# Performance work log

Hardware: AMD Instinct MI355X
Metric: run time of the kernel (lower is better)

The kernel has to match this reference:

```python
import jax, jax.numpy as jnp
import numpy as np

N, E, G = 50000, 800000, 64
IN_NODE, OUT_NODE, IN_EDGE = 16, 20, 16
HID_E, N_ACT, HID_C = 64, 8, 256
BN_EPS = 1e-5


def setup_inputs() -> dict:
    key = jax.random.key(0)
    ks = jax.random.split(key, 12)
    def w(i, shape, scale=0.05):
        return jax.random.normal(ks[i], shape, jnp.float32) * scale
    return {
        "x": jax.random.normal(ks[0], (N, IN_NODE), jnp.float32),
        "edge_attr": jax.random.normal(ks[1], (E, IN_EDGE), jnp.float32),
        "a": jax.random.normal(ks[2], (G, N_ACT), jnp.float32),
        "edge_index": jax.random.randint(ks[3], (2, E), 0, N),
        "batch": jnp.sort(jax.random.randint(ks[4], (N,), 0, G)),
        # edge-conditioning MLP: Lin(16,64) -> BN(64) -> ReLU -> Lin(64, 16*20)
        "W1": w(5, (IN_EDGE, HID_E)), "b1": jnp.zeros((HID_E,), jnp.float32),
        "gamma": jnp.ones((HID_E,), jnp.float32), "beta": jnp.zeros((HID_E,), jnp.float32),
        "W2": w(6, (HID_E, IN_NODE * OUT_NODE)), "b2": jnp.zeros((IN_NODE * OUT_NODE,), jnp.float32),
        # NNConv root weight + bias
        "root_w": w(7, (IN_NODE, OUT_NODE)), "bias": jnp.zeros((OUT_NODE,), jnp.float32),
        # critic head: Lin(20+8,256) -> ReLU -> Lin(256,1)
        "Wc1": w(8, (OUT_NODE + N_ACT, HID_C)), "bc1": jnp.zeros((HID_C,), jnp.float32),
        "Wc2": w(9, (HID_C, 1)), "bc2": jnp.zeros((1,), jnp.float32),
    }


def reference(x, edge_attr, a, W1, b1, gamma, beta, W2, b2, root_w, bias,
              Wc1, bc1, Wc2, bc2, edge_index, batch):
    # edge-conditioning MLP (BatchNorm in training mode: batch stats over edges)
    h = edge_attr @ W1 + b1                              # [E, 64]
    mu = jnp.mean(h, axis=0)
    var = jnp.mean(jnp.square(h - mu), axis=0)           # biased var, as BN fwd
    h = (h - mu) * jax.lax.rsqrt(var + BN_EPS) * gamma + beta
    h = jax.nn.relu(h)
    w_e = (h @ W2 + b2).reshape(E, IN_NODE, OUT_NODE)    # per-edge weight matrix

    src, dst = edge_index[0], edge_index[1]
    msg = jnp.einsum('ei,eio->eo', x[src], w_e)          # gather + per-edge matvec [E, 20]
    aggr = jax.ops.segment_sum(msg, dst, num_segments=N) # scatter-add (NNConv aggr='add')
    out = x @ root_w + aggr + bias                       # [N, 20]

    # global mean pool over graphs
    sums = jax.ops.segment_sum(out, batch, num_segments=G)            # [G, 20]
    cnt = jax.ops.segment_sum(jnp.ones((N, 1), out.dtype), batch, num_segments=G)
    pooled = sums / jnp.maximum(cnt, 1.0)

    z = jnp.concatenate([pooled, a], axis=1)             # [G, 28]
    z = jax.nn.relu(z @ Wc1 + bc1)
    return z @ Wc2 + bc2                                 # [G, 1]
```

## Files before the change

kernel.cpp:

```cpp
#include <hip/hip_runtime.h>


#define E_EDGES   800000
#define N_NODES   50000
#define G_GRAPHS  64
#define EDGE_GRID 6144
#define NGROUPS   50000
#define GSTRIDE   1536
#define NSUP      256
#define STAT_GRID 512
#define QSCALE    131072.0f
#define QINV      (1.0f / 131072.0f)

typedef _Float16 f16x2 __attribute__((ext_vector_type(2)));
typedef _Float16 f16x8 __attribute__((ext_vector_type(8)));
typedef __fp16   fp16x2 __attribute__((ext_vector_type(2)));
typedef float    f32x4 __attribute__((ext_vector_type(4)));
typedef unsigned u32x4 __attribute__((ext_vector_type(4)));

union H2U { f16x2 h; unsigned u; };
union F8U { f16x8 v; f16x2 h2[4]; u32x4 u4; };

__device__ __forceinline__ f16x2 pkrtz(float a, float b) {
  fp16x2 r = __builtin_amdgcn_cvt_pkrtz(a, b);
  return __builtin_bit_cast(f16x2, r);
}

__global__ __launch_bounds__(256) void setup_kernel(
    const float* __restrict__ W2, const float* __restrict__ b2,
    const float* __restrict__ W1, const float* __restrict__ x,
    const float* __restrict__ ea, unsigned* __restrict__ Bbuf,
    unsigned* __restrict__ Bw1, unsigned* __restrict__ xh,
    float* __restrict__ gstatsT)
{
  __shared__ float red[4][272];
  const int b = blockIdx.x, tid = threadIdx.x;
  if (b < STAT_GRID) {
    int lane = tid & 63, wave = tid >> 6;
    int nl = lane & 15, q = lane >> 4;
    int gw = b * 4 + wave;
    f32x4 acc = (f32x4){0.f, 0.f, 0.f, 0.f};
    float ms = 0.f;
    for (int c0 = gw; c0 < E_EDGES / 32; c0 += STAT_GRID * 4) {
      const float* p = ea + (size_t)(c0 * 32 + q * 8) * 16 + nl;
      float v0 = p[0],  v1 = p[16], v2 = p[32], v3 = p[48];
      float v4 = p[64], v5 = p[80], v6 = p[96], v7 = p[112];
      ms += (v0 + v1) + (v2 + v3) + (v4 + v5) + (v6 + v7);
      F8U av;
      av.h2[0] = pkrtz(v0, v1); av.h2[1] = pkrtz(v2, v3);
      av.h2[2] = pkrtz(v4, v5); av.h2[3] = pkrtz(v6, v7);
      acc = __builtin_amdgcn_mfma_f32_16x16x32_f16(av.v, av.v, acc, 0, 0, 0);
    }
    ms += __shfl_xor(ms, 16, 64);
    ms += __shfl_xor(ms, 32, 64);
#pragma unroll
    for (int r = 0; r < 4; ++r) red[wave][(q * 4 + r) * 16 + nl] = acc[r];
    if (q == 0) red[wave][256 + nl] = ms;
    __syncthreads();
    for (int v = tid; v < 272; v += 256)
      gstatsT[(size_t)v * STAT_GRID + b] =
          red[0][v] + red[1][v] + red[2][v] + red[3][v];
  } else if (b < STAT_GRID + 70) {
    int idx = (b - STAT_GRID) * 256 + tid;
    if (idx < 33 * 512) {
      int r = idx & 3, lane = (idx >> 2) & 63, nt = (idx >> 8) & 1,
          s = idx >> 9;
      int q = lane >> 4, nl = lane & 15, n = nt * 16 + nl;
      float v0 = 0.f, v1 = 0.f;
      if (n < 20) {
        if (s < 32) {
          int K0 = s * 32 + q * 8 + 2 * r;
          v0 = W2[(K0 >> 4) * 320 + (K0 & 15) * 20 + n];
          v1 = W2[((K0 + 1) >> 4) * 320 + ((K0 + 1) & 15) * 20 + n];
        } else if (q < 2) {
          int i0 = q * 8 + 2 * r;
          v0 = b2[i0 * 20 + n];
          v1 = b2[(i0 + 1) * 20 + n];
        }
      }
      H2U pk; pk.h = pkrtz(v0, v1);
      Bbuf[idx] = pk.u;
    } else {
      int idx2 = idx - 33 * 512;
      int r = idx2 & 3, lane = (idx2 >> 2) & 63, nt = idx2 >> 8;
      int q = lane >> 4, nl = lane & 15, n = nt * 16 + nl;
      int k0 = q * 8 + 2 * r;
      float v0 = (k0 < 16)     ? W1[k0 * 64 + n]       : 0.f;
      float v1 = (k0 + 1 < 16) ? W1[(k0 + 1) * 64 + n] : 0.f;
      H2U pk; pk.h = pkrtz(v0, v1);
      Bw1[idx2] = pk.u;
    }
  } else {
    int i = (b - STAT_GRID - 70) * 256 + tid;
    if (i < N_NODES * 8) {
      H2U pk; pk.h = pkrtz(x[2 * i], x[2 * i + 1]);
      xh[i] = pk.u;
    }
  }
}

__global__ __launch_bounds__(256) void mid_kernel(
    const float* __restrict__ gstatsT, const float* __restrict__ W1,
    const float* __restrict__ b1, const float* __restrict__ gamma,
    const float* __restrict__ beta, const float* __restrict__ x,
    const int* __restrict__ batch, float* __restrict__ sc,
    float* __restrict__ sh, float* __restrict__ sumx,
    float* __restrict__ cntf)
{
  const int t = threadIdx.x;
  if (blockIdx.x == G_GRAPHS) {
    __shared__ float S[272];
    for (int v = t; v < 272; v += 256) {
      const float* p = gstatsT + (size_t)v * STAT_GRID;
      float s0 = 0.f, s1 = 0.f, s2 = 0.f, s3 = 0.f;
      for (int bb = 0; bb < STAT_GRID; bb += 4) {
        s0 += p[bb]; s1 += p[bb + 1]; s2 += p[bb + 2]; s3 += p[bb + 3];
      }
      S[v] = (s0 + s1) + (s2 + s3);
    }
    __syncthreads();
    if (t < 64) {
      float w[16];
#pragma unroll
      for (int j = 0; j < 16; ++j) w[j] = W1[j * 64 + t];
      const float invE = 1.0f / (float)E_EDGES;
      float mw = 0.f;
#pragma unroll
      for (int j = 0; j < 16; ++j) mw += S[256 + j] * w[j];
      mw *= invE;
      float qf = 0.f;
      for (int j = 0; j < 16; ++j) {
        float tt = 0.f;
#pragma unroll
        for (int j2 = 0; j2 < 16; ++j2) tt += S[j * 16 + j2] * w[j2];
        qf += w[j] * tt;
      }
      qf *= invE;
      float b = b1[t];
      float meanH = mw + b;
      float eh2 = qf + 2.f * b * mw + b * b;
      float var = eh2 - meanH * meanH;
      float s = gamma[t] * rsqrtf(var + 1e-5f);
      sc[t] = s;
      sh[t] = beta[t] + (b - meanH) * s;
    }
  } else {
    int g = blockIdx.x;
    __shared__ int se[2];
    if (t < 2) {
      int key = g + t;
      int lo = 0, hi = N_NODES;
      while (lo < hi) {
        int mid = (lo + hi) >> 1;
        if (batch[mid] < key) lo = mid + 1; else hi = mid;
      }
      se[t] = lo;
    }
    __syncthreads();
    int start = se[0], end = se[1];
    int c = t & 15, rr = t >> 4;
    float s = 0.f;
    for (int n = start + rr; n < end; n += 16) s += x[(size_t)n * 16 + c];
    __shared__ float red[256];
    red[t] = s;
    __syncthreads();
#pragma unroll
    for (int st = 128; st >= 16; st >>= 1) {
      if (t < st) red[t] += red[t + st];
      __syncthreads();
    }
    if (t < 16) sumx[g * 16 + t] = red[t];
    if (t == 0) cntf[g] = (float)(end - start);
  }
}

__global__ __launch_bounds__(64, 3) void edge_kernel(
    const unsigned* __restrict__ xh, const float* __restrict__ ea,
    const int* __restrict__ ei, const int* __restrict__ batch,
    const float* __restrict__ sc, const float* __restrict__ sh,
    const unsigned* __restrict__ Bbuf, const unsigned* __restrict__ Bw1v,
    int* __restrict__ gpartI)
{
  __shared__ unsigned hh[320];
  __shared__ int gacc[1280];
  const int lane = threadIdx.x;
  const int nl = lane & 15, q = lane >> 4;
  const int s = blockIdx.x;
  const int kq = (s >> 3) & 3;
  const int sgroup = ((s >> 5) << 3) | (s & 7);
  const int* srcp = ei;
  const int* dstp = ei + E_EDGES;

  for (int v = lane; v < 1280; v += 64) gacc[v] = 0;

  F8U bb[8][2];
#pragma unroll
  for (int sl = 0; sl < 8; ++sl)
#pragma unroll
    for (int nt = 0; nt < 2; ++nt)
      bb[sl][nt].u4 =
          ((const u32x4*)Bbuf)[((kq * 8 + sl) * 2 + nt) * 64 + lane];
  F8U bx[2];
  if (kq == 3) {
    bx[0].u4 = ((const u32x4*)Bbuf)[64 * 64 + lane];
    bx[1].u4 = ((const u32x4*)Bbuf)[65 * 64 + lane];
  } else {
    bx[0].u4 = (u32x4){0u, 0u, 0u, 0u};
    bx[1].u4 = (u32x4){0u, 0u, 0u, 0u};
  }
  F8U bw1; bw1.u4 = ((const u32x4*)Bw1v)[kq * 64 + lane];
  const float scv = sc[kq * 16 + nl];
  const float shv = sh[kq * 16 + nl];
  const int hrb = (q >> 1) * 20 + nl;
  const int qh = q & 1;

  int g = sgroup;
  f32x4 eaA = (f32x4){0.f,0.f,0.f,0.f}, eaB = eaA;
  u32x4 xp = (u32x4){0u,0u,0u,0u};
  int ge = 0;
  {
    int base = g * 16;
    if (q < 2) {
      const float* p = ea + (size_t)(base + nl) * 16 + q * 8;
      eaA = *(const f32x4*)p;
      eaB = *(const f32x4*)(p + 4);
    }
    int src = srcp[base + nl];
    xp = ((const u32x4*)xh)[src * 2 + qh];
    ge = batch[dstp[base + nl]];
  }

  while (g < NGROUPS) {
    const int gn = g + GSTRIDE;

    {
      F8U aEA;
      if (q < 2) {
        aEA.h2[0] = pkrtz(eaA[0], eaA[1]); aEA.h2[1] = pkrtz(eaA[2], eaA[3]);
        aEA.h2[2] = pkrtz(eaB[0], eaB[1]); aEA.h2[3] = pkrtz(eaB[2], eaB[3]);
      } else {
        aEA.u4 = (u32x4){0u, 0u, 0u, 0u};
      }
      f32x4 hD = __builtin_amdgcn_mfma_f32_16x16x32_f16(
          aEA.v, bw1.v, (f32x4){0.f, 0.f, 0.f, 0.f}, 0, 0, 0);
#pragma unroll
      for (int r = 0; r < 4; ++r) {
        float h = fmaxf(hD[r] * scv + shv, 0.f);
        H2U pk; pk.h = pkrtz(h, h);
        hh[nl * 20 + q * 4 + r] = pk.u;
      }
    }
    F8U xcur; xcur.u4 = xp;
    int gq0 = __shfl(ge, q * 4 + 0, 64);
    int gq1 = __shfl(ge, q * 4 + 1, 64);
    int gq2 = __shfl(ge, q * 4 + 2, 64);
    int gq3 = __shfl(ge, q * 4 + 3, 64);

    f32x4 eaAn = (f32x4){0.f,0.f,0.f,0.f}, eaBn = eaAn;
    u32x4 xpn = (u32x4){0u,0u,0u,0u};
    int gen = 0;
    if (gn < NGROUPS) {
      int base = gn * 16;
      if (q < 2) {
        const float* p = ea + (size_t)(base + nl) * 16 + q * 8;
        eaAn = *(const f32x4*)p;
        eaBn = *(const f32x4*)(p + 4);
      }
      int src = srcp[base + nl];
      xpn = ((const u32x4*)xh)[src * 2 + qh];
      gen = batch[dstp[base + nl]];
    }

    f32x4 acc0 = (f32x4){0.f, 0.f, 0.f, 0.f};
    f32x4 acc1 = (f32x4){0.f, 0.f, 0.f, 0.f};
#pragma unroll
    for (int sl = 0; sl < 8; ++sl) {
      H2U hu; hu.u = hh[hrb + sl * 40];
      F8U av;
      av.h2[0] = hu.h * xcur.h2[0];
      av.h2[1] = hu.h * xcur.h2[1];
      av.h2[2] = hu.h * xcur.h2[2];
      av.h2[3] = hu.h * xcur.h2[3];
      acc0 = __builtin_amdgcn_mfma_f32_16x16x32_f16(av.v, bb[sl][0].v, acc0,
                                                    0, 0, 0);
      acc1 = __builtin_amdgcn_mfma_f32_16x16x32_f16(av.v, bb[sl][1].v, acc1,
                                                    0, 0, 0);
    }
    if (kq == 3) {
      F8U av;
      if (q < 2) av = xcur;
      else       av.u4 = (u32x4){0u, 0u, 0u, 0u};
      acc0 = __builtin_amdgcn_mfma_f32_16x16x32_f16(av.v, bx[0].v, acc0,
                                                    0, 0, 0);
      acc1 = __builtin_amdgcn_mfma_f32_16x16x32_f16(av.v, bx[1].v, acc1,
                                                    0, 0, 0);
    }

    {
      int gi;
      gi = gq0 * 20;
      atomicAdd(&gacc[gi + nl], __float2int_rn(acc0[0] * QSCALE));
      if (nl < 4) atomicAdd(&gacc[gi + 16 + nl], __float2int_rn(acc1[0] * QSCALE));
      gi = gq1 * 20;
      atomicAdd(&gacc[gi + nl], __float2int_rn(acc0[1] * QSCALE));
      if (nl < 4) atomicAdd(&gacc[gi + 16 + nl], __float2int_rn(acc1[1] * QSCALE));
      gi = gq2 * 20;
      atomicAdd(&gacc[gi + nl], __float2int_rn(acc0[2] * QSCALE));
      if (nl < 4) atomicAdd(&gacc[gi + 16 + nl], __float2int_rn(acc1[2] * QSCALE));
      gi = gq3 * 20;
      atomicAdd(&gacc[gi + nl], __float2int_rn(acc0[3] * QSCALE));
      if (nl < 4) atomicAdd(&gacc[gi + 16 + nl], __float2int_rn(acc1[3] * QSCALE));
    }

    g = gn;
    eaA = eaAn; eaB = eaBn; xp = xpn; ge = gen;
  }

  const int ssup = s & (NSUP - 1);
  for (int v = lane; v < 1280; v += 64) {
    int gg = v / 20, o = v - gg * 20;
    atomicAdd(&gpartI[(gg * NSUP + ssup) * 20 + o], gacc[v]);
  }
}

__global__ __launch_bounds__(256) void critic_kernel(
    const int* __restrict__ gpartI, const float* __restrict__ sumx,
    const float* __restrict__ cntf, const float* __restrict__ root_w,
    const float* __restrict__ bias, const float* __restrict__ a,
    const float* __restrict__ Wc1, const float* __restrict__ bc1,
    const float* __restrict__ Wc2, const float* __restrict__ bc2,
    float* __restrict__ out)
{
  int g = blockIdx.x, t = threadIdx.x;
  __shared__ int part[240];
  __shared__ float pooled[20];
  if (t < 240) {
    int col = t % 20, r = t / 20;
    int s = 0;
    const int* gp = gpartI + (size_t)g * NSUP * 20;
    for (int sl = r; sl < NSUP; sl += 12) s += gp[sl * 20 + col];
    part[t] = s;
  }
  __syncthreads();
  if (t < 20) {
    int si = 0;
#pragma unroll
    for (int r = 0; r < 12; ++r) si += part[r * 20 + t];
    float s = (float)si * QINV;
    float cnt = cntf[g];
    float base = bias[t] * cnt;
#pragma unroll
    for (int i = 0; i < 16; ++i) base += sumx[g * 16 + i] * root_w[i * 20 + t];
    pooled[t] = (s + base) / fmaxf(cnt, 1.f);
  }
  __syncthreads();
  float z = bc1[t];
#pragma unroll
  for (int j = 0; j < 20; ++j) z += pooled[j] * Wc1[j * 256 + t];
#pragma unroll
  for (int j = 0; j < 8; ++j) z += a[g * 8 + j] * Wc1[(20 + j) * 256 + t];
  z = fmaxf(z, 0.f);
  float pr = z * Wc2[t];
#pragma unroll
  for (int off = 32; off >= 1; off >>= 1) pr += __shfl_down(pr, off, 64);
  __shared__ float red[4];
  if ((t & 63) == 0) red[t >> 6] = pr;
  __syncthreads();
  if (t == 0) out[g] = red[0] + red[1] + red[2] + red[3] + bc2[0];
}

extern "C" void kernel_launch(void* const* d_in, const int* in_sizes, int n_in,
                              void* d_out, int out_size, void* d_ws,
                              size_t ws_size, hipStream_t stream) {
  const float* x         = (const float*)d_in[0];
  const float* edge_attr = (const float*)d_in[1];
  const float* a         = (const float*)d_in[2];
  const int*   ei        = (const int*)d_in[3];
  const int*   batch     = (const int*)d_in[4];
  const float* W1        = (const float*)d_in[5];
  const float* b1        = (const float*)d_in[6];
  const float* gamma     = (const float*)d_in[7];
  const float* beta      = (const float*)d_in[8];
  const float* W2        = (const float*)d_in[9];
  const float* b2        = (const float*)d_in[10];
  const float* root_w    = (const float*)d_in[11];
  const float* bias      = (const float*)d_in[12];
  const float* Wc1       = (const float*)d_in[13];
  const float* bc1       = (const float*)d_in[14];
  const float* Wc2       = (const float*)d_in[15];
  const float* bc2       = (const float*)d_in[16];
  float* out = (float*)d_out;

  float* wsf     = (float*)d_ws;
  float* sc      = wsf;
  float* sh      = wsf + 64;
  float* sumx    = wsf + 128;
  float* cntf    = wsf + 1152;
  unsigned* Bw1  = (unsigned*)(wsf + 1216);
  unsigned* Bbuf = (unsigned*)(wsf + 2240);
  float* gstatsT = wsf + 19136;
  unsigned* xhp  = (unsigned*)(wsf + 158400);
  int* gpartI    = (int*)(wsf + 558400);

  (void)hipMemsetAsync(gpartI, 0, (size_t)G_GRAPHS * NSUP * 20 * sizeof(int),
                       stream);

  const int XCONV_BLOCKS = (N_NODES * 8 + 255) / 256;
  setup_kernel<<<STAT_GRID + 70 + XCONV_BLOCKS, 256, 0, stream>>>(
      W2, b2, W1, x, edge_attr, Bbuf, Bw1, xhp, gstatsT);
  mid_kernel<<<G_GRAPHS + 1, 256, 0, stream>>>(gstatsT, W1, b1, gamma, beta,
                                               x, batch, sc, sh, sumx, cntf);
  edge_kernel<<<EDGE_GRID, 64, 0, stream>>>(xhp, edge_attr, ei, batch, sc,
                                            sh, Bbuf, Bw1, gpartI);
  critic_kernel<<<G_GRAPHS, 256, 0, stream>>>(gpartI, sumx, cntf, root_w,
                                              bias, a, Wc1, bc1, Wc2, bc2,
                                              out);
}
```

Measured before the change: 252.4 us.

## Software-pipeline edge kernel with double-buffered hidden tile and split MFMA chains

Restructures the edge loop so the hidden activations for the next group are computed one iteration ahead into a double-buffered LDS tile, and global loads are prefetched two groups ahead. The main MFMA accumulation is split into two independent accumulator chains per output tile to shorten dependency chains. Float-to-int quantization uses a magic-number add trick instead of a round conversion. This costs more registers and LDS, which may cut occupancy under the 3-waves bound.

Measured after the change: 239.5 us. 5.1% less time.

```diff
diff --git a/kernel.cpp b/kernel.cpp
--- a/kernel.cpp
+++ b/kernel.cpp
@@ -24,6 +24,11 @@
 __device__ __forceinline__ f16x2 pkrtz(float a, float b) {
   fp16x2 r = __builtin_amdgcn_cvt_pkrtz(a, b);
   return __builtin_bit_cast(f16x2, r);
+}
+
+__device__ __forceinline__ int q17(float x) {
+  float r = __builtin_fmaf(x, QSCALE, 12582912.0f);
+  return __builtin_bit_cast(int, r) - 0x4B400000;
 }
 
 __global__ __launch_bounds__(256) void setup_kernel(
@@ -181,7 +186,7 @@
     const unsigned* __restrict__ Bbuf, const unsigned* __restrict__ Bw1v,
     int* __restrict__ gpartI)
 {
-  __shared__ unsigned hh[320];
+  __shared__ unsigned hh[640];
   __shared__ int gacc[1280];
   const int lane = threadIdx.x;
   const int nl = lane & 15, q = lane >> 4;
@@ -215,105 +220,158 @@
   const int qh = q & 1;
 
   int g = sgroup;
-  f32x4 eaA = (f32x4){0.f,0.f,0.f,0.f}, eaB = eaA;
-  u32x4 xp = (u32x4){0u,0u,0u,0u};
-  int ge = 0;
+  f32x4 eaAn = (f32x4){0.f,0.f,0.f,0.f}, eaBn = eaAn;
+  f32x4 eaA2 = eaAn, eaB2 = eaAn;
+  u32x4 xp = (u32x4){0u,0u,0u,0u}, xpn = xp, xp2 = xp;
+  int ge = 0, gen = 0, ge2 = 0;
   {
     int base = g * 16;
     if (q < 2) {
       const float* p = ea + (size_t)(base + nl) * 16 + q * 8;
-      eaA = *(const f32x4*)p;
-      eaB = *(const f32x4*)(p + 4);
+      eaAn = *(const f32x4*)p;
+      eaBn = *(const f32x4*)(p + 4);
     }
     int src = srcp[base + nl];
     xp = ((const u32x4*)xh)[src * 2 + qh];
     ge = batch[dstp[base + nl]];
   }
+  {
+    F8U aEA;
+    if (q < 2) {
+      aEA.h2[0] = pkrtz(eaAn[0], eaAn[1]); aEA.h2[1] = pkrtz(eaAn[2], eaAn[3]);
+      aEA.h2[2] = pkrtz(eaBn[0], eaBn[1]); aEA.h2[3] = pkrtz(eaBn[2], eaBn[3]);
+    } else {
+      aEA.u4 = (u32x4){0u, 0u, 0u, 0u};
+    }
+    f32x4 hD = __builtin_amdgcn_mfma_f32_16x16x32_f16(
+        aEA.v, bw1.v, (f32x4){0.f, 0.f, 0.f, 0.f}, 0, 0, 0);
+#pragma unroll
+    for (int r = 0; r < 4; ++r) {
+      float h = fmaxf(hD[r] * scv + shv, 0.f);
+      H2U pk; pk.h = pkrtz(h, h);
+      hh[nl * 20 + q * 4 + r] = pk.u;
+    }
+  }
+  if (g + GSTRIDE < NGROUPS) {
+    int base = (g + GSTRIDE) * 16;
+    if (q < 2) {
+      const float* p = ea + (size_t)(base + nl) * 16 + q * 8;
+      eaAn = *(const f32x4*)p;
+      eaBn = *(const f32x4*)(p + 4);
+    }
+    int src = srcp[base + nl];
+    xpn = ((const u32x4*)xh)[src * 2 + qh];
+    gen = batch[dstp[base + nl]];
+  }
+  int cur = 0;
 
   while (g < NGROUPS) {
-    const int gn = g + GSTRIDE;
-
-    {
+    const int gn = g + GSTRIDE, gnn = gn + GSTRIDE;
+    const int hb = cur * 320 + hrb;
+
+    unsigned hu[8];
+#pragma unroll
+    for (int sl = 0; sl < 8; ++sl) hu[sl] = hh[hb + sl * 40];
+    const int gq0 = __shfl(ge, q * 4 + 0, 64);
+    const int gq1 = __shfl(ge, q * 4 + 1, 64);
+    const int gq2 = __shfl(ge, q * 4 + 2, 64);
+    const int gq3 = __shfl(ge, q * 4 + 3, 64);
+
+    f32x4 hDn = (f32x4){0.f, 0.f, 0.f, 0.f};
+    const bool hvalid = (gn < NGROUPS);
+    if (hvalid) {
       F8U aEA;
       if (q < 2) {
-        aEA.h2[0] = pkrtz(eaA[0], eaA[1]); aEA.h2[1] = pkrtz(eaA[2], eaA[3]);
-        aEA.h2[2] = pkrtz(eaB[0], eaB[1]); aEA.h2[3] = pkrtz(eaB[2], eaB[3]);
+        aEA.h2[0] = pkrtz(eaAn[0], eaAn[1]);
+        aEA.h2[1] = pkrtz(eaAn[2], eaAn[3]);
+        aEA.h2[2] = pkrtz(eaBn[0], eaBn[1]);
+        aEA.h2[3] = pkrtz(eaBn[2], eaBn[3]);
       } else {
         aEA.u4 = (u32x4){0u, 0u, 0u, 0u};
       }
-      f32x4 hD = __builtin_amdgcn_mfma_f32_16x16x32_f16(
+      hDn = __builtin_amdgcn_mfma_f32_16x16x32_f16(
           aEA.v, bw1.v, (f32x4){0.f, 0.f, 0.f, 0.f}, 0, 0, 0);
-#pragma unroll
-      for (int r = 0; r < 4; ++r) {
-        float h = fmaxf(hD[r] * scv + shv, 0.f);
-        H2U pk; pk.h = pkrtz(h, h);
-        hh[nl * 20 + q * 4 + r] = pk.u;
-      }
-    }
-    F8U xcur; xcur.u4 = xp;
-    int gq0 = __shfl(ge, q * 4 + 0, 64);
-    int gq1 = __shfl(ge, q * 4 + 1, 64);
-    int gq2 = __shfl(ge, q * 4 + 2, 64);
-    int gq3 = __shfl(ge, q * 4 + 3, 64);
-
-    f32x4 eaAn = (f32x4){0.f,0.f,0.f,0.f}, eaBn = eaAn;
-    u32x4 xpn = (u32x4){0u,0u,0u,0u};
-    int gen = 0;
-    if (gn < NGROUPS) {
-      int base = gn * 16;
+    }
+
+    if (gnn < NGROUPS) {
+      int base = gnn * 16;
       if (q < 2) {
         const float* p = ea + (size_t)(base + nl) * 16 + q * 8;
-        eaAn = *(const f32x4*)p;
-        eaBn = *(const f32x4*)(p + 4);
+        eaA2 = *(const f32x4*)p;
+        eaB2 = *(const f32x4*)(p + 4);
       }
       int src = srcp[base + nl];
-      xpn = ((const u32x4*)xh)[src * 2 + qh];
-      gen = batch[dstp[base + nl]];
-    }
-
-    f32x4 acc0 = (f32x4){0.f, 0.f, 0.f, 0.f};
-    f32x4 acc1 = (f32x4){0.f, 0.f, 0.f, 0.f};
-#pragma unroll
-    for (int sl = 0; sl < 8; ++sl) {
-      H2U hu; hu.u = hh[hrb + sl * 40];
-      F8U av;
-      av.h2[0] = hu.h * xcur.h2[0];
-      av.h2[1] = hu.h * xcur.h2[1];
-      av.h2[2] = hu.h * xcur.h2[2];
-      av.h2[3] = hu.h * xcur.h2[3];
-      acc0 = __builtin_amdgcn_mfma_f32_16x16x32_f16(av.v, bb[sl][0].v, acc0,
-                                                    0, 0, 0);
-      acc1 = __builtin_amdgcn_mfma_f32_16x16x32_f16(av.v, bb[sl][1].v, acc1,
-                                                    0, 0, 0);
+      xp2 = ((const u32x4*)xh)[src * 2 + qh];
+      ge2 = batch[dstp[base + nl]];
+    }
+
+    F8U xcur; xcur.u4 = xp;
+    f32x4 a00 = (f32x4){0.f, 0.f, 0.f, 0.f};
+    f32x4 a01 = a00, a10 = a00, a11 = a00;
+#pragma unroll
+    for (int sl = 0; sl < 8; sl += 2) {
+      H2U u0; u0.u = hu[sl];
+      H2U u1; u1.u = hu[sl + 1];
+      F8U av0, av1;
+      av0.h2[0] = u0.h * xcur.h2[0];
+      av0.h2[1] = u0.h * xcur.h2[1];
+      av0.h2[2] = u0.h * xcur.h2[2];
+      av0.h2[3] = u0.h * xcur.h2[3];
+      av1.h2[0] = u1.h * xcur.h2[0];
+      av1.h2[1] = u1.h * xcur.h2[1];
+      av1.h2[2] = u1.h * xcur.h2[2];
+      av1.h2[3] = u1.h * xcur.h2[3];
+      a00 = __builtin_amdgcn_mfma_f32_16x16x32_f16(av0.v, bb[sl][0].v, a00,
+                                                   0, 0, 0);
+      a10 = __builtin_amdgcn_mfma_f32_16x16x32_f16(av0.v, bb[sl][1].v, a10,
+                                                   0, 0, 0);
+      a01 = __builtin_amdgcn_mfma_f32_16x16x32_f16(av1.v, bb[sl + 1][0].v,
+                                                   a01, 0, 0, 0);
+      a11 = __builtin_amdgcn_mfma_f32_16x16x32_f16(av1.v, bb[sl + 1][1].v,
+                                                   a11, 0, 0, 0);
     }
     if (kq == 3) {
       F8U av;
       if (q < 2) av = xcur;
       else       av.u4 = (u32x4){0u, 0u, 0u, 0u};
-      acc0 = __builtin_amdgcn_mfma_f32_16x16x32_f16(av.v, bx[0].v, acc0,
-                                                    0, 0, 0);
-      acc1 = __builtin_amdgcn_mfma_f32_16x16x32_f16(av.v, bx[1].v, acc1,
-                                                    0, 0, 0);
+      a00 = __builtin_amdgcn_mfma_f32_16x16x32_f16(av.v, bx[0].v, a00,
+                                                   0, 0, 0);
+      a10 = __builtin_amdgcn_mfma_f32_16x16x32_f16(av.v, bx[1].v, a10,
+                                                   0, 0, 0);
+    }
+    const f32x4 acc0 = a00 + a01;
+    const f32x4 acc1 = a10 + a11;
+
+    if (hvalid) {
+      const int hw = (cur ^ 1) * 320 + nl * 20 + q * 4;
+#pragma unroll
+      for (int r = 0; r < 4; ++r) {
+        float h = fmaxf(hDn[r] * scv + shv, 0.f);
+        H2U pk; pk.h = pkrtz(h, h);
+        hh[hw + r] = pk.u;
+      }
     }
 
     {
       int gi;
       gi = gq0 * 20;
-      atomicAdd(&gacc[gi + nl], __float2int_rn(acc0[0] * QSCALE));
-      if (nl < 4) atomicAdd(&gacc[gi + 16 + nl], __float2int_rn(acc1[0] * QSCALE));
+      atomicAdd(&gacc[gi + nl], q17(acc0[0]));
+      if (nl < 4) atomicAdd(&gacc[gi + 16 + nl], q17(acc1[0]));
       gi = gq1 * 20;
-      atomicAdd(&gacc[gi + nl], __float2int_rn(acc0[1] * QSCALE));
-      if (nl < 4) atomicAdd(&gacc[gi + 16 + nl], __float2int_rn(acc1[1] * QSCALE));
+      atomicAdd(&gacc[gi + nl], q17(acc0[1]));
+      if (nl < 4) atomicAdd(&gacc[gi + 16 + nl], q17(acc1[1]));
       gi = gq2 * 20;
-      atomicAdd(&gacc[gi + nl], __float2int_rn(acc0[2] * QSCALE));
-      if (nl < 4) atomicAdd(&gacc[gi + 16 + nl], __float2int_rn(acc1[2] * QSCALE));
+      atomicAdd(&gacc[gi + nl], q17(acc0[2]));
+      if (nl < 4) atomicAdd(&gacc[gi + 16 + nl], q17(acc1[2]));
       gi = gq3 * 20;
-      atomicAdd(&gacc[gi + nl], __float2int_rn(acc0[3] * QSCALE));
-      if (nl < 4) atomicAdd(&gacc[gi + 16 + nl], __float2int_rn(acc1[3] * QSCALE));
-    }
-
-    g = gn;
-    eaA = eaAn; eaB = eaBn; xp = xpn; ge = gen;
+      atomicAdd(&gacc[gi + nl], q17(acc0[3]));
+      if (nl < 4) atomicAdd(&gacc[gi + 16 + nl], q17(acc1[3]));
+    }
+
+    g = gn; cur ^= 1;
+    xp = xpn; ge = gen;
+    xpn = xp2; gen = ge2;
+    eaAn = eaA2; eaBn = eaB2;
   }
 
   const int ssup = s & (NSUP - 1);
```
